# Performance work log

Measured on AMD Instinct MI355X. Metric: run time of the kernel, lower is better.

Reference implementation:

```python
import jax, jax.numpy as jnp
import numpy as np

N = 100000
E = 640000
IN_DIM = 128
HID = 128
NUM_REL = 8


def _rgcn_layer(x, rel_w, root_w, bias, src, dst, edge_type, num_nodes):
    # PyG RGCNConv: out = x @ root + bias + sum_r mean_{edges of rel r into v}(x_src) @ W_r
    out = x @ root_w + bias
    x_src = x[src]  # [E, d_in]
    for r in range(NUM_REL):
        w = (edge_type == r).astype(x.dtype)  # [E]
        msg_sum = jax.ops.segment_sum(x_src * w[:, None], dst, num_segments=num_nodes)
        cnt = jax.ops.segment_sum(w, dst, num_segments=num_nodes)
        agg = msg_sum / jnp.maximum(cnt, 1.0)[:, None]  # mean aggregation per relation
        out = out + agg @ rel_w[r]
    return out


def setup_inputs() -> dict:
    key = jax.random.key(0)
    ks = jax.random.split(key, 10)
    x = jax.random.normal(ks[0], (N, IN_DIM), dtype=jnp.float32)
    edge_index = jax.random.randint(ks[1], (2, E), 0, N, dtype=jnp.int64)
    edge_type = jax.random.randint(ks[2], (E,), 0, NUM_REL, dtype=jnp.int64)
    s1 = 1.0 / np.sqrt(IN_DIM)
    s2 = 1.0 / np.sqrt(HID)
    rel_w1 = jax.random.uniform(ks[3], (NUM_REL, IN_DIM, HID), jnp.float32, -s1, s1)
    root_w1 = jax.random.uniform(ks[4], (IN_DIM, HID), jnp.float32, -s1, s1)
    b1 = jnp.zeros((HID,), jnp.float32)
    rel_w2 = jax.random.uniform(ks[5], (NUM_REL, HID, HID), jnp.float32, -s2, s2)
    root_w2 = jax.random.uniform(ks[6], (HID, HID), jnp.float32, -s2, s2)
    b2 = jnp.zeros((HID,), jnp.float32)
    return {"x": x, "edge_index": edge_index, "edge_type": edge_type,
            "rel_w1": rel_w1, "root_w1": root_w1, "b1": b1,
            "rel_w2": rel_w2, "root_w2": root_w2, "b2": b2}


def reference(x, edge_index, edge_type, rel_w1, root_w1, b1, rel_w2, root_w2, b2):
    src, dst = edge_index[0], edge_index[1]
    h = _rgcn_layer(x, rel_w1, root_w1, b1, src, dst, edge_type, N)
    h = jax.nn.relu(h)  # dropout p=0.0 -> identity
    h = _rgcn_layer(h, rel_w2, root_w2, b2, src, dst, edge_type, N)
    h = jax.nn.relu(h)
    return h
```

## Files before the change

### kernel.cpp

```cpp
#include <hip/hip_runtime.h>
#include <hip/hip_bf16.h>

#define NN 100000
#define EE 640000
#define DD 128
#define RR 8
#define K8 (NN * RR)
#define NSB1 25
#define NSB2 196
#define GBMAX 11571

typedef __attribute__((ext_vector_type(8))) short short8;
typedef __attribute__((ext_vector_type(4))) float floatx4;
typedef __attribute__((ext_vector_type(4))) unsigned int uint4v;

__device__ __forceinline__ unsigned short f2bf(float f) {
  unsigned int u = __float_as_uint(f);
  u += 0x7FFFu + ((u >> 16) & 1u);
  return (unsigned short)(u >> 16);
}
__device__ __forceinline__ unsigned int pk2bf(float a, float b) {
  __hip_bfloat162 h = __float22bfloat162_rn(make_float2(a, b));
  unsigned int u;
  __builtin_memcpy(&u, &h, 4);
  return u;
}
__device__ __forceinline__ float bflo(unsigned int u) { return __uint_as_float(u << 16); }
__device__ __forceinline__ float bfhi(unsigned int u) { return __uint_as_float(u & 0xFFFF0000u); }

__global__ __launch_bounds__(256) void xb_prep(
    const float* __restrict__ x, unsigned int* __restrict__ xb)
{
  int g = blockIdx.x * 256 + threadIdx.x;
  int v = g >> 4, seg = g & 15;
  const float4* s4 = (const float4*)(x + (size_t)v * 128 + seg * 8);
  float4 a = s4[0], b = s4[1];
  uint4v o;
  o[0] = pk2bf(a.x, a.y); o[1] = pk2bf(a.z, a.w);
  o[2] = pk2bf(b.x, b.y); o[3] = pk2bf(b.z, b.w);
  *(uint4v*)(xb + (size_t)v * 64 + seg * 4) = o;
}

__global__ __launch_bounds__(256) void w_prep_all(
    const float* __restrict__ rel1, const float* __restrict__ root1,
    const float* __restrict__ rel2, const float* __restrict__ root2,
    unsigned short* __restrict__ wt)
{
  int id = blockIdx.x * 256 + threadIdx.x;
  int set = id >= 147456;
  int rem = id - set * 147456;
  int r = rem >> 14, n = (rem >> 7) & 127, k = rem & 127;
  const float* rel = set ? rel2 : rel1;
  const float* root = set ? root2 : root1;
  float v = (r < RR) ? rel[((size_t)r * DD + k) * DD + n] : root[(size_t)k * DD + n];
  wt[id] = f2bf(v);
}

__global__ __launch_bounds__(256) void count_all(
    const int* __restrict__ ei, const int* __restrict__ et,
    int* __restrict__ cntd, int* __restrict__ cntdr, int* __restrict__ cntsr)
{
  int e = blockIdx.x * 256 + threadIdx.x;
  int src = ei[e], dst = ei[EE + e], r = et[e];
  atomicAdd(&cntd[dst], 1);
  atomicAdd(&cntdr[dst * RR + r], 1);
  atomicAdd(&cntsr[r * NN + src], 1);
}

__global__ __launch_bounds__(256) void scan_a(
    const int4* __restrict__ c4, int n4, int mode, int* __restrict__ bsum)
{
  int t = threadIdx.x;
  int s = 0;
#pragma unroll
  for (int i = 0; i < 4; ++i) {
    int idx = blockIdx.x * 1024 + i * 256 + t;
    if (idx < n4) {
      int4 v = c4[idx];
      if (mode) s += (v.x > 0) + (v.y > 0) + (v.z > 0) + (v.w > 0);
      else      s += v.x + v.y + v.z + v.w;
    }
  }
  __shared__ int wsum[4];
  for (int d = 32; d; d >>= 1) s += __shfl_xor(s, d, 64);
  if ((t & 63) == 0) wsum[t >> 6] = s;
  __syncthreads();
  if (t == 0) bsum[blockIdx.x] = wsum[0] + wsum[1] + wsum[2] + wsum[3];
}

__global__ void scan_b(const int* __restrict__ bsum, int nsb,
                       int* __restrict__ bbase, int* __restrict__ tot)
{
  int lane = threadIdx.x;
  int v[4]; int s = 0;
#pragma unroll
  for (int i = 0; i < 4; ++i) {
    int idx = lane * 4 + i;
    v[i] = (idx < nsb) ? bsum[idx] : 0; s += v[i];
  }
  int inc = s;
  for (int d = 1; d < 64; d <<= 1) {
    int o = __shfl_up(inc, d, 64);
    if (lane >= d) inc += o;
  }
  int running = inc - s;
#pragma unroll
  for (int i = 0; i < 4; ++i) {
    int idx = lane * 4 + i;
    if (idx < nsb) { bbase[idx] = running; running += v[i]; }
  }
  if (lane == 63 && tot != nullptr) tot[0] = inc;
}

__global__ __launch_bounds__(256) void scan_c(
    const int* __restrict__ cnt, const int* __restrict__ bbase, int n, int mode,
    int* __restrict__ out0, int* __restrict__ out1, int* __restrict__ ubp)
{
  int t = threadIdx.x;
  int base = blockIdx.x * 4096 + t * 16;
  int v[16]; int s = 0;
#pragma unroll
  for (int i = 0; i < 16; ++i) {
    int idx = base + i;
    v[i] = (idx < n) ? cnt[idx] : 0;
    s += mode ? (v[i] > 0) : v[i];
  }
  int lane = t & 63, wid = t >> 6;
  int inc = s;
  for (int d = 1; d < 64; d <<= 1) {
    int o = __shfl_up(inc, d, 64);
    if (lane >= d) inc += o;
  }
  __shared__ int wsum[4];
  if (lane == 63) wsum[wid] = inc;
  __syncthreads();
  int wb = 0;
  for (int w = 0; w < wid; ++w) wb += wsum[w];
  int running = bbase[blockIdx.x] + wb + (inc - s);
#pragma unroll
  for (int i = 0; i < 16; ++i) {
    int idx = base + i;
    if (idx < n) {
      if (mode) {
        if (idx % NN == 0) ubp[idx / NN] = running;
        out0[idx] = (v[i] > 0) ? running : -1;
        running += (v[i] > 0);
      } else {
        out0[idx] = running; out1[idx] = running; running += v[i];
      }
    }
  }
  if (!mode && blockIdx.x == 0 && t == 0) out0[n] = EE;
}

__global__ void pb_kernel(const int* __restrict__ ub, const int* __restrict__ tot,
                          int* __restrict__ pb)
{
  if (threadIdx.x == 0) {
    int base = 0;
    for (int r = 0; r < RR; ++r) {
      pb[r] = base;
      int hi = (r == RR - 1) ? tot[0] : ub[r + 1];
      int u = hi - ub[r];
      base += (u + 63) & ~63;
    }
    pb[8] = base;
    pb[9] = base + ((NN + 63) & ~63);
  }
}

__global__ __launch_bounds__(256) void fix_kernel(
    int* __restrict__ pidx, const int* __restrict__ ub,
    const int* __restrict__ pb, int* __restrict__ ysrc)
{
  int key = blockIdx.x * 256 + threadIdx.x;
  int g = pidx[key];
  if (g < 0) return;
  int r = key / NN, src = key - r * NN;
  int y = pb[r] + (g - ub[r]);
  pidx[key] = y;
  ysrc[y] = src;
}

__global__ __launch_bounds__(256) void place2(
    const int* __restrict__ ei, const int* __restrict__ et,
    const int* __restrict__ cntdr, const int* __restrict__ pidx,
    int* __restrict__ rowfill, int2* __restrict__ recs)
{
  int e = blockIdx.x * 256 + threadIdx.x;
  int src = ei[e], dst = ei[EE + e], r = et[e];
  int slot = atomicAdd(&rowfill[dst], 1);
  float s = 1.0f / (float)max(cntdr[dst * RR + r], 1);
  int2 rec; rec.x = pidx[r * NN + src]; rec.y = __float_as_int(s);
  recs[slot] = rec;
}

__global__ __launch_bounds__(256, 3) void gemm_y(
    const unsigned int* __restrict__ Xb,
    const unsigned short* __restrict__ Wt,
    const int* __restrict__ ysrc,
    const int* __restrict__ pb,
    unsigned int* __restrict__ Ypk)
{
  const int yrow0 = blockIdx.x * 64;
  if (yrow0 >= pb[9]) return;
  int r = 8;
#pragma unroll
  for (int rr = 0; rr < 8; ++rr) if (yrow0 < pb[rr + 1]) { r = rr; break; }

  __shared__ unsigned short As[64 * 128];
  const int tid = threadIdx.x;
  const int wave = tid >> 6, lane = tid & 63;
  const int quad = lane >> 4, mr = lane & 15;
  const int pb8 = pb[8];

  {
    int row = tid >> 2, q = tid & 3;
    int yrow = yrow0 + row;
    int src;
    if (r < RR) src = ysrc[yrow];
    else { src = yrow - pb8; if (src >= NN) src = 0; }
    const uint4v* xs = (const uint4v*)(Xb + (size_t)src * 64 + q * 16);
#pragma unroll
    for (int c = 0; c < 4; ++c) {
      uint4v v = xs[c];
      int pos = (q * 32 + c * 8 + (row & 15) * 8) & 127;
      *(uint4v*)&As[row * 128 + pos] = v;
    }
  }
  const unsigned short* wr = Wt + (size_t)r * 16384 + (size_t)(wave * 32 + mr) * 128 + quad * 8;
  short8 b0[4], b1[4];
#pragma unroll
  for (int ks = 0; ks < 4; ++ks) {
    b0[ks] = *(const short8*)(wr + ks * 32);
    b1[ks] = *(const short8*)(wr + 16 * 128 + ks * 32);
  }
  __syncthreads();

  floatx4 acc[4][2];
#pragma unroll
  for (int mi = 0; mi < 4; ++mi) {
    acc[mi][0] = (floatx4){0.f, 0.f, 0.f, 0.f};
    acc[mi][1] = (floatx4){0.f, 0.f, 0.f, 0.f};
  }
#pragma unroll
  for (int ks = 0; ks < 4; ++ks) {
    short8 a[4];
#pragma unroll
    for (int mi = 0; mi < 4; ++mi)
      a[mi] = *(const short8*)&As[(mi * 16 + mr) * 128 +
                                  ((ks * 32 + quad * 8 + mr * 8) & 127)];
#pragma unroll
    for (int mi = 0; mi < 4; ++mi) {
      acc[mi][0] = __builtin_amdgcn_mfma_f32_16x16x32_bf16(a[mi], b0[ks], acc[mi][0], 0, 0, 0);
      acc[mi][1] = __builtin_amdgcn_mfma_f32_16x16x32_bf16(a[mi], b1[ks], acc[mi][1], 0, 0, 0);
    }
  }
#pragma unroll
  for (int mi = 0; mi < 4; ++mi)
#pragma unroll
    for (int rg = 0; rg < 4; ++rg)
      Ypk[(size_t)(yrow0 + mi * 16 + quad * 4 + rg) * 64 + wave * 16 + mr] =
          pk2bf(acc[mi][0][rg], acc[mi][1][rg]);
}

__global__ __launch_bounds__(256) void aggregate(
    const unsigned int* __restrict__ Ypk,
    const int* __restrict__ rowptr,
    const int2* __restrict__ recs,
    const int* __restrict__ pb,
    const float* __restrict__ bias,
    void* __restrict__ outp, int out_bf16)
{
  int gid = blockIdx.x * 256 + threadIdx.x;
  int v = gid >> 3, o = gid & 7;
  int c0 = 32 * (o >> 1) + 8 * (o & 1);
  int pb8 = pb[8];

  float lo[8], hi[8];
  {
    const uint4v* rp = (const uint4v*)(Ypk + (size_t)(pb8 + v) * 64 + o * 8);
    uint4v u0 = rp[0], u1 = rp[1];
    unsigned um[8];
    *(uint4v*)&um[0] = u0; *(uint4v*)&um[4] = u1;
#pragma unroll
    for (int j = 0; j < 8; ++j) {
      lo[j] = bias[c0 + j] + bflo(um[j]);
      hi[j] = bias[c0 + 16 + j] + bfhi(um[j]);
    }
  }

  int beg = rowptr[v], end = rowptr[v + 1];
  if (beg < end) {
    int2 rec = recs[beg];
    const uint4v* yp = (const uint4v*)(Ypk + (size_t)rec.x * 64 + o * 8);
    uint4v c0v = yp[0], c1v = yp[1];
    for (int e = beg; e < end; ++e) {
      int2 nrec = rec;
      uint4v n0 = c0v, n1 = c1v;
      if (e + 1 < end) {
        nrec = recs[e + 1];
        const uint4v* np = (const uint4v*)(Ypk + (size_t)nrec.x * 64 + o * 8);
        n0 = np[0]; n1 = np[1];
      }
      float s = __int_as_float(rec.y);
      unsigned um[8];
      *(uint4v*)&um[0] = c0v; *(uint4v*)&um[4] = c1v;
#pragma unroll
      for (int j = 0; j < 8; ++j) {
        lo[j] = fmaf(s, bflo(um[j]), lo[j]);
        hi[j] = fmaf(s, bfhi(um[j]), hi[j]);
      }
      rec = nrec; c0v = n0; c1v = n1;
    }
  }

#pragma unroll
  for (int j = 0; j < 8; ++j) {
    lo[j] = fmaxf(lo[j], 0.f);
    hi[j] = fmaxf(hi[j], 0.f);
  }

  if (out_bf16) {
    unsigned int* h = (unsigned int*)outp;
    uint4v wl, wh;
#pragma unroll
    for (int t = 0; t < 4; ++t) {
      wl[t] = pk2bf(lo[2 * t], lo[2 * t + 1]);
      wh[t] = pk2bf(hi[2 * t], hi[2 * t + 1]);
    }
    *(uint4v*)&h[(size_t)v * 64 + c0 / 2] = wl;
    *(uint4v*)&h[(size_t)v * 64 + c0 / 2 + 8] = wh;
  } else {
    float* out = (float*)outp;
    float4* dl = (float4*)(out + (size_t)v * 128 + c0);
    float4* dh = (float4*)(out + (size_t)v * 128 + c0 + 16);
    dl[0] = make_float4(lo[0], lo[1], lo[2], lo[3]);
    dl[1] = make_float4(lo[4], lo[5], lo[6], lo[7]);
    dh[0] = make_float4(hi[0], hi[1], hi[2], hi[3]);
    dh[1] = make_float4(hi[4], hi[5], hi[6], hi[7]);
  }
}

extern "C" void kernel_launch(void* const* d_in, const int* in_sizes, int n_in,
                              void* d_out, int out_size, void* d_ws, size_t ws_size,
                              hipStream_t stream) {
  const float* x       = (const float*)d_in[0];
  const int*   ei      = (const int*)d_in[1];
  const int*   et      = (const int*)d_in[2];
  const float* rel_w1  = (const float*)d_in[3];
  const float* root_w1 = (const float*)d_in[4];
  const float* b1      = (const float*)d_in[5];
  const float* rel_w2  = (const float*)d_in[6];
  const float* root_w2 = (const float*)d_in[7];
  const float* b2      = (const float*)d_in[8];

  char* ws = (char*)d_ws;
  size_t off = 0;
  auto alloc = [&](size_t bytes) { char* p = ws + off; off = (off + bytes + 255) & ~(size_t)255; return p; };
  unsigned int*   Ypk   = (unsigned int*)alloc((size_t)(EE + NN + 1024) * 64 * 4);
  unsigned int*   Xb    = (unsigned int*)alloc((size_t)NN * 64 * 4);
  unsigned int*   h1    = (unsigned int*)alloc((size_t)NN * 64 * 4);
  unsigned short* Wt    = (unsigned short*)alloc((size_t)2 * 9 * DD * DD * 2);
  int*            cntd  = (int*)alloc((size_t)NN * 4);
  int*            cntdr = (int*)alloc((size_t)K8 * 4);
  int*            cntsr = (int*)alloc((size_t)K8 * 4);
  int*            ysrc  = (int*)alloc((size_t)(EE + 1024) * 4);
  char*           zend  = ws + off;
  int*            rowptr= (int*)alloc((size_t)(NN + 1) * 4);
  int*            rowfill=(int*)alloc((size_t)NN * 4);
  int*            pidx  = (int*)alloc((size_t)K8 * 4);
  int2*           recs  = (int2*)alloc((size_t)EE * 8);
  int*            bsum1 = (int*)alloc((size_t)NSB1 * 4);
  int*            bbase1= (int*)alloc((size_t)NSB1 * 4);
  int*            bsum2 = (int*)alloc((size_t)NSB2 * 4);
  int*            bbase2= (int*)alloc((size_t)NSB2 * 4);
  int*            ub    = (int*)alloc(64);
  int*            pb    = (int*)alloc(64);
  int*            Ptot  = (int*)alloc(64);

  hipMemsetAsync(cntd, 0, (size_t)(zend - (char*)cntd), stream);

  xb_prep<<<(NN * 16) / 256, 256, 0, stream>>>(x, Xb);
  w_prep_all<<<(2 * 9 * DD * DD) / 256, 256, 0, stream>>>(rel_w1, root_w1, rel_w2, root_w2, Wt);
  count_all<<<EE / 256, 256, 0, stream>>>(ei, et, cntd, cntdr, cntsr);

  scan_a<<<NSB1, 256, 0, stream>>>((const int4*)cntd, NN / 4, 0, bsum1);
  scan_b<<<1, 64, 0, stream>>>(bsum1, NSB1, bbase1, nullptr);
  scan_c<<<NSB1, 256, 0, stream>>>(cntd, bbase1, NN, 0, rowptr, rowfill, nullptr);

  scan_a<<<NSB2, 256, 0, stream>>>((const int4*)cntsr, K8 / 4, 1, bsum2);
  scan_b<<<1, 64, 0, stream>>>(bsum2, NSB2, bbase2, Ptot);
  scan_c<<<NSB2, 256, 0, stream>>>(cntsr, bbase2, K8, 1, pidx, nullptr, ub);
  pb_kernel<<<1, 64, 0, stream>>>(ub, Ptot, pb);
  fix_kernel<<<K8 / 256, 256, 0, stream>>>(pidx, ub, pb, ysrc);

  place2<<<EE / 256, 256, 0, stream>>>(ei, et, cntdr, pidx, rowfill, recs);

  const int AB = (NN * 8) / 256;

  gemm_y<<<GBMAX, 256, 0, stream>>>(Xb, Wt, ysrc, pb, Ypk);
  aggregate<<<AB, 256, 0, stream>>>(Ypk, rowptr, recs, pb, b1, h1, 1);
  gemm_y<<<GBMAX, 256, 0, stream>>>(h1, Wt + (size_t)9 * DD * DD, ysrc, pb, Ypk);
  aggregate<<<AB, 256, 0, stream>>>(Ypk, rowptr, recs, pb, b2, d_out, 0);
}
```

Baseline: 435.8 us.

## Build per-(dst,rel) CSR via atomic ranks and byte usage flags

The count pass now records each edge's atomic rank within its (dst, relation) bucket and marks used (relation, src) pairs with byte flags, replacing three atomic counters with one atomic plus a plain store. A scan over the dst×relation counts builds a finer row pointer, so edge placement becomes deterministic (offset plus rank) instead of a second atomic pass, and records end up grouped by relation inside each destination row. The usage scan reads packed bytes instead of int counters. In exchange, the destination-count scan grows from 100K to 800K entries and an extra per-edge rank array is written and read.

```diff
diff --git a/kernel.cpp b/kernel.cpp
--- a/kernel.cpp
+++ b/kernel.cpp
@@ -6,7 +6,6 @@
 #define DD 128
 #define RR 8
 #define K8 (NN * RR)
-#define NSB1 25
 #define NSB2 196
 #define GBMAX 11571
 
@@ -58,28 +57,24 @@
 
 __global__ __launch_bounds__(256) void count_all(
     const int* __restrict__ ei, const int* __restrict__ et,
-    int* __restrict__ cntd, int* __restrict__ cntdr, int* __restrict__ cntsr)
+    int* __restrict__ cntdr, unsigned char* __restrict__ used,
+    int* __restrict__ erank)
 {
   int e = blockIdx.x * 256 + threadIdx.x;
   int src = ei[e], dst = ei[EE + e], r = et[e];
-  atomicAdd(&cntd[dst], 1);
-  atomicAdd(&cntdr[dst * RR + r], 1);
-  atomicAdd(&cntsr[r * NN + src], 1);
+  erank[e] = atomicAdd(&cntdr[dst * RR + r], 1);
+  used[r * NN + src] = 1;
 }
 
 __global__ __launch_bounds__(256) void scan_a(
-    const int4* __restrict__ c4, int n4, int mode, int* __restrict__ bsum)
+    const int4* __restrict__ c4, int n4, int* __restrict__ bsum)
 {
   int t = threadIdx.x;
   int s = 0;
 #pragma unroll
   for (int i = 0; i < 4; ++i) {
     int idx = blockIdx.x * 1024 + i * 256 + t;
-    if (idx < n4) {
-      int4 v = c4[idx];
-      if (mode) s += (v.x > 0) + (v.y > 0) + (v.z > 0) + (v.w > 0);
-      else      s += v.x + v.y + v.z + v.w;
-    }
+    if (idx < n4) { int4 v = c4[idx]; s += v.x + v.y + v.z + v.w; }
   }
   __shared__ int wsum[4];
   for (int d = 32; d; d >>= 1) s += __shfl_xor(s, d, 64);
@@ -88,6 +83,28 @@
   if (t == 0) bsum[blockIdx.x] = wsum[0] + wsum[1] + wsum[2] + wsum[3];
 }
 
+__global__ __launch_bounds__(256) void scan_a_u8(
+    const uint4v* __restrict__ c, int n16, int* __restrict__ bsum)
+{
+  int t = threadIdx.x;
+  int idx = blockIdx.x * 256 + t;
+  int s = 0;
+  if (idx < n16) {
+    uint4v v = c[idx];
+#pragma unroll
+    for (int w = 0; w < 4; ++w) {
+      unsigned u = v[w];
+      s += ((u & 0x000000FFu) ? 1 : 0) + ((u & 0x0000FF00u) ? 1 : 0)
+         + ((u & 0x00FF0000u) ? 1 : 0) + ((u & 0xFF000000u) ? 1 : 0);
+    }
+  }
+  __shared__ int wsum[4];
+  for (int d = 32; d; d >>= 1) s += __shfl_xor(s, d, 64);
+  if ((t & 63) == 0) wsum[t >> 6] = s;
+  __syncthreads();
+  if (t == 0) bsum[blockIdx.x] = wsum[0] + wsum[1] + wsum[2] + wsum[3];
+}
+
 __global__ void scan_b(const int* __restrict__ bsum, int nsb,
                        int* __restrict__ bbase, int* __restrict__ tot)
 {
@@ -113,8 +130,8 @@
 }
 
 __global__ __launch_bounds__(256) void scan_c(
-    const int* __restrict__ cnt, const int* __restrict__ bbase, int n, int mode,
-    int* __restrict__ out0, int* __restrict__ out1, int* __restrict__ ubp)
+    const int* __restrict__ cnt, const int* __restrict__ bbase, int n,
+    int* __restrict__ out0)
 {
   int t = threadIdx.x;
   int base = blockIdx.x * 4096 + t * 16;
@@ -123,7 +140,7 @@
   for (int i = 0; i < 16; ++i) {
     int idx = base + i;
     v[i] = (idx < n) ? cnt[idx] : 0;
-    s += mode ? (v[i] > 0) : v[i];
+    s += v[i];
   }
   int lane = t & 63, wid = t >> 6;
   int inc = s;
@@ -140,17 +157,53 @@
 #pragma unroll
   for (int i = 0; i < 16; ++i) {
     int idx = base + i;
+    if (idx < n) { out0[idx] = running; running += v[i]; }
+  }
+  if (blockIdx.x == 0 && t == 0) out0[n] = EE;
+}
+
+__global__ __launch_bounds__(256) void scan_c_u8(
+    const unsigned char* __restrict__ used, const int* __restrict__ bbase, int n,
+    int* __restrict__ out0, int* __restrict__ ubp)
+{
+  int t = threadIdx.x;
+  int base = blockIdx.x * 4096 + t * 16;
+  int v[16]; int s = 0;
+  if (base < n) {
+    uint4v u = *(const uint4v*)(used + base);
+    unsigned um[4]; *(uint4v*)um = u;
+#pragma unroll
+    for (int w = 0; w < 4; ++w)
+#pragma unroll
+      for (int b = 0; b < 4; ++b) {
+        v[w * 4 + b] = ((um[w] >> (8 * b)) & 0xFFu) != 0;
+        s += v[w * 4 + b];
+      }
+  } else {
+#pragma unroll
+    for (int i = 0; i < 16; ++i) v[i] = 0;
+  }
+  int lane = t & 63, wid = t >> 6;
+  int inc = s;
+  for (int d = 1; d < 64; d <<= 1) {
+    int o = __shfl_up(inc, d, 64);
+    if (lane >= d) inc += o;
+  }
+  __shared__ int wsum[4];
+  if (lane == 63) wsum[wid] = inc;
+  __syncthreads();
+  int wb = 0;
+  for (int w = 0; w < wid; ++w) wb += wsum[w];
+  int running = bbase[blockIdx.x] + wb + (inc - s);
+#pragma unroll
+  for (int i = 0; i < 16; ++i) {
+    int idx = base + i;
     if (idx < n) {
-      if (mode) {
-        if (idx % NN == 0) ubp[idx / NN] = running;
-        out0[idx] = (v[i] > 0) ? running : -1;
-        running += (v[i] > 0);
-      } else {
-        out0[idx] = running; out1[idx] = running; running += v[i];
-      }
-    }
-  }
-  if (!mode && blockIdx.x == 0 && t == 0) out0[n] = EE;
+      if (idx % NN == 0) ubp[idx / NN] = running;
+      out0[idx] = v[i] ? running : -1;
+      running += v[i];
+    }
+  }
 }
 
 __global__ void pb_kernel(const int* __restrict__ ub, const int* __restrict__ tot,
@@ -184,13 +237,15 @@
 
 __global__ __launch_bounds__(256) void place2(
     const int* __restrict__ ei, const int* __restrict__ et,
-    const int* __restrict__ cntdr, const int* __restrict__ pidx,
-    int* __restrict__ rowfill, int2* __restrict__ recs)
+    const int* __restrict__ rowptr_dr, const int* __restrict__ pidx,
+    const int* __restrict__ erank, int2* __restrict__ recs)
 {
   int e = blockIdx.x * 256 + threadIdx.x;
   int src = ei[e], dst = ei[EE + e], r = et[e];
-  int slot = atomicAdd(&rowfill[dst], 1);
-  float s = 1.0f / (float)max(cntdr[dst * RR + r], 1);
+  int k = dst * RR + r;
+  int b0 = rowptr_dr[k], b1 = rowptr_dr[k + 1];
+  int slot = b0 + erank[e];
+  float s = 1.0f / (float)max(b1 - b0, 1);
   int2 rec; rec.x = pidx[r * NN + src]; rec.y = __float_as_int(s);
   recs[slot] = rec;
 }
@@ -290,7 +345,7 @@
     }
   }
 
-  int beg = rowptr[v], end = rowptr[v + 1];
+  int beg = rowptr[v * RR], end = rowptr[v * RR + RR];
   if (beg < end) {
     int2 rec = recs[beg];
     const uint4v* yp = (const uint4v*)(Ypk + (size_t)rec.x * 64 + o * 8);
@@ -362,45 +417,44 @@
   unsigned int*   Xb    = (unsigned int*)alloc((size_t)NN * 64 * 4);
   unsigned int*   h1    = (unsigned int*)alloc((size_t)NN * 64 * 4);
   unsigned short* Wt    = (unsigned short*)alloc((size_t)2 * 9 * DD * DD * 2);
-  int*            cntd  = (int*)alloc((size_t)NN * 4);
   int*            cntdr = (int*)alloc((size_t)K8 * 4);
-  int*            cntsr = (int*)alloc((size_t)K8 * 4);
+  unsigned char*  used  = (unsigned char*)alloc((size_t)K8);
   int*            ysrc  = (int*)alloc((size_t)(EE + 1024) * 4);
   char*           zend  = ws + off;
-  int*            rowptr= (int*)alloc((size_t)(NN + 1) * 4);
-  int*            rowfill=(int*)alloc((size_t)NN * 4);
+  int*            rowptr_dr = (int*)alloc((size_t)(K8 + 1) * 4);
+  int*            erank = (int*)alloc((size_t)EE * 4);
   int*            pidx  = (int*)alloc((size_t)K8 * 4);
   int2*           recs  = (int2*)alloc((size_t)EE * 8);
-  int*            bsum1 = (int*)alloc((size_t)NSB1 * 4);
-  int*            bbase1= (int*)alloc((size_t)NSB1 * 4);
-  int*            bsum2 = (int*)alloc((size_t)NSB2 * 4);
-  int*            bbase2= (int*)alloc((size_t)NSB2 * 4);
+  int*            bsumA = (int*)alloc((size_t)NSB2 * 4);
+  int*            bbaseA= (int*)alloc((size_t)NSB2 * 4);
+  int*            bsumB = (int*)alloc((size_t)NSB2 * 4);
+  int*            bbaseB= (int*)alloc((size_t)NSB2 * 4);
   int*            ub    = (int*)alloc(64);
   int*            pb    = (int*)alloc(64);
   int*            Ptot  = (int*)alloc(64);
 
-  hipMemsetAsync(cntd, 0, (size_t)(zend - (char*)cntd), stream);
+  hipMemsetAsync(cntdr, 0, (size_t)(zend - (char*)cntdr), stream);
 
   xb_prep<<<(NN * 16) / 256, 256, 0, stream>>>(x, Xb);
   w_prep_all<<<(2 * 9 * DD * DD) / 256, 256, 0, stream>>>(rel_w1, root_w1, rel_w2, root_w2, Wt);
-  count_all<<<EE / 256, 256, 0, stream>>>(ei, et, cntd, cntdr, cntsr);
-
-  scan_a<<<NSB1, 256, 0, stream>>>((const int4*)cntd, NN / 4, 0, bsum1);
-  scan_b<<<1, 64, 0, stream>>>(bsum1, NSB1, bbase1, nullptr);
-  scan_c<<<NSB1, 256, 0, stream>>>(cntd, bbase1, NN, 0, rowptr, rowfill, nullptr);
-
-  scan_a<<<NSB2, 256, 0, stream>>>((const int4*)cntsr, K8 / 4, 1, bsum2);
-  scan_b<<<1, 64, 0, stream>>>(bsum2, NSB2, bbase2, Ptot);
-  scan_c<<<NSB2, 256, 0, stream>>>(cntsr, bbase2, K8, 1, pidx, nullptr, ub);
+  count_all<<<EE / 256, 256, 0, stream>>>(ei, et, cntdr, used, erank);
+
+  scan_a<<<NSB2, 256, 0, stream>>>((const int4*)cntdr, K8 / 4, bsumA);
+  scan_b<<<1, 64, 0, stream>>>(bsumA, NSB2, bbaseA, nullptr);
+  scan_c<<<NSB2, 256, 0, stream>>>(cntdr, bbaseA, K8, rowptr_dr);
+
+  scan_a_u8<<<NSB2, 256, 0, stream>>>((const uint4v*)used, K8 / 16, bsumB);
+  scan_b<<<1, 64, 0, stream>>>(bsumB, NSB2, bbaseB, Ptot);
+  scan_c_u8<<<NSB2, 256, 0, stream>>>(used, bbaseB, K8, pidx, ub);
   pb_kernel<<<1, 64, 0, stream>>>(ub, Ptot, pb);
   fix_kernel<<<K8 / 256, 256, 0, stream>>>(pidx, ub, pb, ysrc);
 
-  place2<<<EE / 256, 256, 0, stream>>>(ei, et, cntdr, pidx, rowfill, recs);
+  place2<<<EE / 256, 256, 0, stream>>>(ei, et, rowptr_dr, pidx, erank, recs);
 
   const int AB = (NN * 8) / 256;
 
   gemm_y<<<GBMAX, 256, 0, stream>>>(Xb, Wt, ysrc, pb, Ypk);
-  aggregate<<<AB, 256, 0, stream>>>(Ypk, rowptr, recs, pb, b1, h1, 1);
+  aggregate<<<AB, 256, 0, stream>>>(Ypk, rowptr_dr, recs, pb, b1, h1, 1);
   gemm_y<<<GBMAX, 256, 0, stream>>>(h1, Wt + (size_t)9 * DD * DD, ysrc, pb, Ypk);
-  aggregate<<<AB, 256, 0, stream>>>(Ypk, rowptr, recs, pb, b2, d_out, 0);
-}
+  aggregate<<<AB, 256, 0, stream>>>(Ypk, rowptr_dr, recs, pb, b2, d_out, 0);
+}
```

Result: faster. 377.2 us (-13.4%).

## Fuse per-relation mean aggregation with GEMM; aggregate-then-transform per node tile

Applied to the files above, without the earlier changes.

Replaces the transform-then-gather scheme (a GEMM over every unique (relation, source) row into a large Y buffer, then an edge aggregation pass) with one fused kernel per layer. For a tile of 64 destination nodes, that kernel gathers and averages the bf16 source features for each relation into shared memory and multiplies by W_r with MFMA, accumulating all relations plus the root term in registers. The preprocessing becomes a single (relation, dst) CSR built from atomic ranks, which drops several scan, fix and placement kernels along with the large intermediate Y buffer and its traffic. In exchange, the gather is serialized per relation inside each block, there are nine MFMA rounds per tile, and the layer-2 weight rows are permuted to match the h1 bf16 packing.

```diff
diff --git a/kernel.cpp b/kernel.cpp
--- a/kernel.cpp
+++ b/kernel.cpp
@@ -6,9 +6,8 @@
 #define DD 128
 #define RR 8
 #define K8 (NN * RR)
-#define NSB1 25
 #define NSB2 196
-#define GBMAX 11571
+#define NB 1563
 
 typedef __attribute__((ext_vector_type(8))) short short8;
 typedef __attribute__((ext_vector_type(4))) float floatx4;
@@ -50,36 +49,35 @@
   int set = id >= 147456;
   int rem = id - set * 147456;
   int r = rem >> 14, n = (rem >> 7) & 127, k = rem & 127;
+  int kk = k;
+  if (set) {
+    int u = k >> 1, w2 = u >> 4, m2 = u & 15;
+    kk = w2 * 32 + m2 + ((k & 1) << 4);
+  }
   const float* rel = set ? rel2 : rel1;
   const float* root = set ? root2 : root1;
-  float v = (r < RR) ? rel[((size_t)r * DD + k) * DD + n] : root[(size_t)k * DD + n];
+  float v = (r < RR) ? rel[((size_t)r * DD + kk) * DD + n] : root[(size_t)kk * DD + n];
   wt[id] = f2bf(v);
 }
 
 __global__ __launch_bounds__(256) void count_all(
     const int* __restrict__ ei, const int* __restrict__ et,
-    int* __restrict__ cntd, int* __restrict__ cntdr, int* __restrict__ cntsr)
+    int* __restrict__ cnt, int* __restrict__ erank)
 {
   int e = blockIdx.x * 256 + threadIdx.x;
-  int src = ei[e], dst = ei[EE + e], r = et[e];
-  atomicAdd(&cntd[dst], 1);
-  atomicAdd(&cntdr[dst * RR + r], 1);
-  atomicAdd(&cntsr[r * NN + src], 1);
+  int dst = ei[EE + e], r = et[e];
+  erank[e] = atomicAdd(&cnt[r * NN + dst], 1);
 }
 
 __global__ __launch_bounds__(256) void scan_a(
-    const int4* __restrict__ c4, int n4, int mode, int* __restrict__ bsum)
+    const int4* __restrict__ c4, int n4, int* __restrict__ bsum)
 {
   int t = threadIdx.x;
   int s = 0;
 #pragma unroll
   for (int i = 0; i < 4; ++i) {
     int idx = blockIdx.x * 1024 + i * 256 + t;
-    if (idx < n4) {
-      int4 v = c4[idx];
-      if (mode) s += (v.x > 0) + (v.y > 0) + (v.z > 0) + (v.w > 0);
-      else      s += v.x + v.y + v.z + v.w;
-    }
+    if (idx < n4) { int4 v = c4[idx]; s += v.x + v.y + v.z + v.w; }
   }
   __shared__ int wsum[4];
   for (int d = 32; d; d >>= 1) s += __shfl_xor(s, d, 64);
@@ -89,7 +87,7 @@
 }
 
 __global__ void scan_b(const int* __restrict__ bsum, int nsb,
-                       int* __restrict__ bbase, int* __restrict__ tot)
+                       int* __restrict__ bbase)
 {
   int lane = threadIdx.x;
   int v[4]; int s = 0;
@@ -109,12 +107,11 @@
     int idx = lane * 4 + i;
     if (idx < nsb) { bbase[idx] = running; running += v[i]; }
   }
-  if (lane == 63 && tot != nullptr) tot[0] = inc;
 }
 
 __global__ __launch_bounds__(256) void scan_c(
-    const int* __restrict__ cnt, const int* __restrict__ bbase, int n, int mode,
-    int* __restrict__ out0, int* __restrict__ out1, int* __restrict__ ubp)
+    const int* __restrict__ cnt, const int* __restrict__ bbase, int n,
+    int* __restrict__ out0)
 {
   int t = threadIdx.x;
   int base = blockIdx.x * 4096 + t * 16;
@@ -123,7 +120,7 @@
   for (int i = 0; i < 16; ++i) {
     int idx = base + i;
     v[i] = (idx < n) ? cnt[idx] : 0;
-    s += mode ? (v[i] > 0) : v[i];
+    s += v[i];
   }
   int lane = t & 63, wid = t >> 6;
   int inc = s;
@@ -140,102 +137,66 @@
 #pragma unroll
   for (int i = 0; i < 16; ++i) {
     int idx = base + i;
-    if (idx < n) {
-      if (mode) {
-        if (idx % NN == 0) ubp[idx / NN] = running;
-        out0[idx] = (v[i] > 0) ? running : -1;
-        running += (v[i] > 0);
-      } else {
-        out0[idx] = running; out1[idx] = running; running += v[i];
-      }
-    }
-  }
-  if (!mode && blockIdx.x == 0 && t == 0) out0[n] = EE;
-}
-
-__global__ void pb_kernel(const int* __restrict__ ub, const int* __restrict__ tot,
-                          int* __restrict__ pb)
-{
-  if (threadIdx.x == 0) {
-    int base = 0;
-    for (int r = 0; r < RR; ++r) {
-      pb[r] = base;
-      int hi = (r == RR - 1) ? tot[0] : ub[r + 1];
-      int u = hi - ub[r];
-      base += (u + 63) & ~63;
-    }
-    pb[8] = base;
-    pb[9] = base + ((NN + 63) & ~63);
-  }
-}
-
-__global__ __launch_bounds__(256) void fix_kernel(
-    int* __restrict__ pidx, const int* __restrict__ ub,
-    const int* __restrict__ pb, int* __restrict__ ysrc)
-{
-  int key = blockIdx.x * 256 + threadIdx.x;
-  int g = pidx[key];
-  if (g < 0) return;
-  int r = key / NN, src = key - r * NN;
-  int y = pb[r] + (g - ub[r]);
-  pidx[key] = y;
-  ysrc[y] = src;
-}
-
-__global__ __launch_bounds__(256) void place2(
+    if (idx < n) { out0[idx] = running; running += v[i]; }
+  }
+  if (blockIdx.x == 0 && t == 0) out0[n] = EE;
+}
+
+__global__ __launch_bounds__(256) void place(
     const int* __restrict__ ei, const int* __restrict__ et,
-    const int* __restrict__ cntdr, const int* __restrict__ pidx,
-    int* __restrict__ rowfill, int2* __restrict__ recs)
+    const int* __restrict__ rowptr, const int* __restrict__ erank,
+    int* __restrict__ recs)
 {
   int e = blockIdx.x * 256 + threadIdx.x;
   int src = ei[e], dst = ei[EE + e], r = et[e];
-  int slot = atomicAdd(&rowfill[dst], 1);
-  float s = 1.0f / (float)max(cntdr[dst * RR + r], 1);
-  int2 rec; rec.x = pidx[r * NN + src]; rec.y = __float_as_int(s);
-  recs[slot] = rec;
-}
-
-__global__ __launch_bounds__(256, 3) void gemm_y(
+  recs[rowptr[r * NN + dst] + erank[e]] = src;
+}
+
+#define MFMA_ROUND()                                                          \
+  {                                                                           \
+    __syncthreads();                                                          \
+    _Pragma("unroll")                                                         \
+    for (int ks = 0; ks < 4; ++ks) {                                          \
+      short8 a[4];                                                            \
+      _Pragma("unroll")                                                       \
+      for (int mi = 0; mi < 4; ++mi)                                          \
+        a[mi] = *(const short8*)&As[(mi * 16 + mr) * 128 +                    \
+                                    ((ks * 32 + quad * 8 + mr * 8) & 127)];   \
+      _Pragma("unroll")                                                       \
+      for (int mi = 0; mi < 4; ++mi) {                                        \
+        acc[mi][0] = __builtin_amdgcn_mfma_f32_16x16x32_bf16(                 \
+            a[mi], b0[ks], acc[mi][0], 0, 0, 0);                              \
+        acc[mi][1] = __builtin_amdgcn_mfma_f32_16x16x32_bf16(                 \
+            a[mi], b1[ks], acc[mi][1], 0, 0, 0);                              \
+      }                                                                       \
+    }                                                                         \
+    __syncthreads();                                                          \
+  }
+
+__global__ __launch_bounds__(256, 3) void gemm_agg(
     const unsigned int* __restrict__ Xb,
     const unsigned short* __restrict__ Wt,
-    const int* __restrict__ ysrc,
-    const int* __restrict__ pb,
-    unsigned int* __restrict__ Ypk)
-{
-  const int yrow0 = blockIdx.x * 64;
-  if (yrow0 >= pb[9]) return;
-  int r = 8;
-#pragma unroll
-  for (int rr = 0; rr < 8; ++rr) if (yrow0 < pb[rr + 1]) { r = rr; break; }
-
+    const int* __restrict__ rowptr,
+    const int* __restrict__ recs,
+    const float* __restrict__ bias,
+    void* __restrict__ outp, int out_bf16)
+{
+  const int v0 = blockIdx.x * 64;
   __shared__ unsigned short As[64 * 128];
+  __shared__ int Rp[8 * 65];
+
   const int tid = threadIdx.x;
   const int wave = tid >> 6, lane = tid & 63;
   const int quad = lane >> 4, mr = lane & 15;
-  const int pb8 = pb[8];
-
-  {
-    int row = tid >> 2, q = tid & 3;
-    int yrow = yrow0 + row;
-    int src;
-    if (r < RR) src = ysrc[yrow];
-    else { src = yrow - pb8; if (src >= NN) src = 0; }
-    const uint4v* xs = (const uint4v*)(Xb + (size_t)src * 64 + q * 16);
-#pragma unroll
-    for (int c = 0; c < 4; ++c) {
-      uint4v v = xs[c];
-      int pos = (q * 32 + c * 8 + (row & 15) * 8) & 127;
-      *(uint4v*)&As[row * 128 + pos] = v;
-    }
-  }
-  const unsigned short* wr = Wt + (size_t)r * 16384 + (size_t)(wave * 32 + mr) * 128 + quad * 8;
-  short8 b0[4], b1[4];
-#pragma unroll
-  for (int ks = 0; ks < 4; ++ks) {
-    b0[ks] = *(const short8*)(wr + ks * 32);
-    b1[ks] = *(const short8*)(wr + 16 * 128 + ks * 32);
-  }
-  __syncthreads();
+  const int g = lane >> 3, li = lane & 7;
+  const uint4v* Xb4 = (const uint4v*)Xb;
+  unsigned int* Asu = (unsigned int*)As;
+
+  for (int id = tid; id < 520; id += 256) {
+    int r = id / 65, j = id - r * 65;
+    int k = r * NN + v0 + j;
+    Rp[id] = rowptr[min(k, K8)];
+  }
 
   floatx4 acc[4][2];
 #pragma unroll
@@ -243,103 +204,114 @@
     acc[mi][0] = (floatx4){0.f, 0.f, 0.f, 0.f};
     acc[mi][1] = (floatx4){0.f, 0.f, 0.f, 0.f};
   }
-#pragma unroll
-  for (int ks = 0; ks < 4; ++ks) {
-    short8 a[4];
-#pragma unroll
-    for (int mi = 0; mi < 4; ++mi)
-      a[mi] = *(const short8*)&As[(mi * 16 + mr) * 128 +
-                                  ((ks * 32 + quad * 8 + mr * 8) & 127)];
-#pragma unroll
-    for (int mi = 0; mi < 4; ++mi) {
-      acc[mi][0] = __builtin_amdgcn_mfma_f32_16x16x32_bf16(a[mi], b0[ks], acc[mi][0], 0, 0, 0);
-      acc[mi][1] = __builtin_amdgcn_mfma_f32_16x16x32_bf16(a[mi], b1[ks], acc[mi][1], 0, 0, 0);
-    }
-  }
+  __syncthreads();
+
+#pragma unroll 1
+  for (int r = 0; r < 8; ++r) {
+    const unsigned short* wr =
+        Wt + (size_t)r * 16384 + (size_t)(wave * 32 + mr) * 128 + quad * 8;
+    short8 b0[4], b1[4];
+#pragma unroll
+    for (int ks = 0; ks < 4; ++ks) {
+      b0[ks] = *(const short8*)(wr + ks * 32);
+      b1[ks] = *(const short8*)(wr + 16 * 128 + ks * 32);
+    }
+
+#pragma unroll
+    for (int half = 0; half < 2; ++half) {
+      int d = wave * 16 + half * 8 + g;
+      int v = v0 + d;
+      int b = Rp[r * 65 + d];
+      int e = (v < NN) ? Rp[r * 65 + d + 1] : b;
+      int cnt = e - b;
+      int recv = (li < cnt) ? recs[b + li] : 0;
+      float f[16];
+#pragma unroll
+      for (int j = 0; j < 16; ++j) f[j] = 0.f;
+
+      int srcC = __shfl(recv, (g << 3), 64);
+      uint4v u0c{}, u1c{};
+      if (cnt > 0) {
+        const uint4v* xp = Xb4 + (size_t)srcC * 16 + li * 2;
+        u0c = xp[0]; u1c = xp[1];
+      }
+      for (int t = 0; __any(t < cnt); ++t) {
+        int tn = t + 1;
+        int srcN = __shfl(recv, (g << 3) + (tn & 7), 64);
+        bool actN = tn < cnt;
+        if (actN && tn >= 8) srcN = recs[b + tn];
+        uint4v u0n{}, u1n{};
+        if (actN) {
+          const uint4v* xp = Xb4 + (size_t)srcN * 16 + li * 2;
+          u0n = xp[0]; u1n = xp[1];
+        }
+        if (t < cnt) {
+          unsigned um[8];
+          *(uint4v*)&um[0] = u0c; *(uint4v*)&um[4] = u1c;
+#pragma unroll
+          for (int m = 0; m < 8; ++m) {
+            f[2 * m]     += bflo(um[m]);
+            f[2 * m + 1] += bfhi(um[m]);
+          }
+        }
+        u0c = u0n; u1c = u1n;
+      }
+      float sc = 1.0f / (float)max(cnt, 1);
+      int rot = (d & 15) * 4;
+      uint4v o0, o1;
+#pragma unroll
+      for (int m = 0; m < 4; ++m)
+        o0[m] = pk2bf(f[2 * m] * sc, f[2 * m + 1] * sc);
+#pragma unroll
+      for (int m = 0; m < 4; ++m)
+        o1[m] = pk2bf(f[8 + 2 * m] * sc, f[9 + 2 * m] * sc);
+      *(uint4v*)&Asu[d * 64 + ((li * 8 + rot) & 63)] = o0;
+      *(uint4v*)&Asu[d * 64 + ((li * 8 + rot + 4) & 63)] = o1;
+    }
+    MFMA_ROUND();
+  }
+
+  {
+    const unsigned short* wr =
+        Wt + (size_t)8 * 16384 + (size_t)(wave * 32 + mr) * 128 + quad * 8;
+    short8 b0[4], b1[4];
+#pragma unroll
+    for (int ks = 0; ks < 4; ++ks) {
+      b0[ks] = *(const short8*)(wr + ks * 32);
+      b1[ks] = *(const short8*)(wr + 16 * 128 + ks * 32);
+    }
+    int row = tid >> 2, q = tid & 3;
+    int v = v0 + row;
+    int src = (v < NN) ? v : 0;
+    const uint4v* xs = Xb4 + (size_t)src * 16 + q * 4;
+#pragma unroll
+    for (int c = 0; c < 4; ++c) {
+      uint4v vv = xs[c];
+      int pos = (q * 16 + c * 4 + (row & 15) * 4) & 63;
+      *(uint4v*)&Asu[row * 64 + pos] = vv;
+    }
+    MFMA_ROUND();
+  }
+
+  float bia0 = bias[wave * 32 + mr], bia1 = bias[wave * 32 + 16 + mr];
 #pragma unroll
   for (int mi = 0; mi < 4; ++mi)
 #pragma unroll
-    for (int rg = 0; rg < 4; ++rg)
-      Ypk[(size_t)(yrow0 + mi * 16 + quad * 4 + rg) * 64 + wave * 16 + mr] =
-          pk2bf(acc[mi][0][rg], acc[mi][1][rg]);
-}
-
-__global__ __launch_bounds__(256) void aggregate(
-    const unsigned int* __restrict__ Ypk,
-    const int* __restrict__ rowptr,
-    const int2* __restrict__ recs,
-    const int* __restrict__ pb,
-    const float* __restrict__ bias,
-    void* __restrict__ outp, int out_bf16)
-{
-  int gid = blockIdx.x * 256 + threadIdx.x;
-  int v = gid >> 3, o = gid & 7;
-  int c0 = 32 * (o >> 1) + 8 * (o & 1);
-  int pb8 = pb[8];
-
-  float lo[8], hi[8];
-  {
-    const uint4v* rp = (const uint4v*)(Ypk + (size_t)(pb8 + v) * 64 + o * 8);
-    uint4v u0 = rp[0], u1 = rp[1];
-    unsigned um[8];
-    *(uint4v*)&um[0] = u0; *(uint4v*)&um[4] = u1;
-#pragma unroll
-    for (int j = 0; j < 8; ++j) {
-      lo[j] = bias[c0 + j] + bflo(um[j]);
-      hi[j] = bias[c0 + 16 + j] + bfhi(um[j]);
-    }
-  }
-
-  int beg = rowptr[v], end = rowptr[v + 1];
-  if (beg < end) {
-    int2 rec = recs[beg];
-    const uint4v* yp = (const uint4v*)(Ypk + (size_t)rec.x * 64 + o * 8);
-    uint4v c0v = yp[0], c1v = yp[1];
-    for (int e = beg; e < end; ++e) {
-      int2 nrec = rec;
-      uint4v n0 = c0v, n1 = c1v;
-      if (e + 1 < end) {
-        nrec = recs[e + 1];
-        const uint4v* np = (const uint4v*)(Ypk + (size_t)nrec.x * 64 + o * 8);
-        n0 = np[0]; n1 = np[1];
+    for (int rg = 0; rg < 4; ++rg) {
+      int row = mi * 16 + quad * 4 + rg;
+      int v = v0 + row;
+      if (v < NN) {
+        float c0 = fmaxf(acc[mi][0][rg] + bia0, 0.f);
+        float c1 = fmaxf(acc[mi][1][rg] + bia1, 0.f);
+        if (out_bf16) {
+          ((unsigned int*)outp)[(size_t)v * 64 + wave * 16 + mr] = pk2bf(c0, c1);
+        } else {
+          float* o = (float*)outp;
+          o[(size_t)v * 128 + wave * 32 + mr] = c0;
+          o[(size_t)v * 128 + wave * 32 + 16 + mr] = c1;
+        }
       }
-      float s = __int_as_float(rec.y);
-      unsigned um[8];
-      *(uint4v*)&um[0] = c0v; *(uint4v*)&um[4] = c1v;
-#pragma unroll
-      for (int j = 0; j < 8; ++j) {
-        lo[j] = fmaf(s, bflo(um[j]), lo[j]);
-        hi[j] = fmaf(s, bfhi(um[j]), hi[j]);
-      }
-      rec = nrec; c0v = n0; c1v = n1;
-    }
-  }
-
-#pragma unroll
-  for (int j = 0; j < 8; ++j) {
-    lo[j] = fmaxf(lo[j], 0.f);
-    hi[j] = fmaxf(hi[j], 0.f);
-  }
-
-  if (out_bf16) {
-    unsigned int* h = (unsigned int*)outp;
-    uint4v wl, wh;
-#pragma unroll
-    for (int t = 0; t < 4; ++t) {
-      wl[t] = pk2bf(lo[2 * t], lo[2 * t + 1]);
-      wh[t] = pk2bf(hi[2 * t], hi[2 * t + 1]);
-    }
-    *(uint4v*)&h[(size_t)v * 64 + c0 / 2] = wl;
-    *(uint4v*)&h[(size_t)v * 64 + c0 / 2 + 8] = wh;
-  } else {
-    float* out = (float*)outp;
-    float4* dl = (float4*)(out + (size_t)v * 128 + c0);
-    float4* dh = (float4*)(out + (size_t)v * 128 + c0 + 16);
-    dl[0] = make_float4(lo[0], lo[1], lo[2], lo[3]);
-    dl[1] = make_float4(lo[4], lo[5], lo[6], lo[7]);
-    dh[0] = make_float4(hi[0], hi[1], hi[2], hi[3]);
-    dh[1] = make_float4(hi[4], hi[5], hi[6], hi[7]);
-  }
+    }
 }
 
 extern "C" void kernel_launch(void* const* d_in, const int* in_sizes, int n_in,
@@ -358,49 +330,28 @@
   char* ws = (char*)d_ws;
   size_t off = 0;
   auto alloc = [&](size_t bytes) { char* p = ws + off; off = (off + bytes + 255) & ~(size_t)255; return p; };
-  unsigned int*   Ypk   = (unsigned int*)alloc((size_t)(EE + NN + 1024) * 64 * 4);
   unsigned int*   Xb    = (unsigned int*)alloc((size_t)NN * 64 * 4);
   unsigned int*   h1    = (unsigned int*)alloc((size_t)NN * 64 * 4);
   unsigned short* Wt    = (unsigned short*)alloc((size_t)2 * 9 * DD * DD * 2);
-  int*            cntd  = (int*)alloc((size_t)NN * 4);
-  int*            cntdr = (int*)alloc((size_t)K8 * 4);
-  int*            cntsr = (int*)alloc((size_t)K8 * 4);
-  int*            ysrc  = (int*)alloc((size_t)(EE + 1024) * 4);
-  char*           zend  = ws + off;
-  int*            rowptr= (int*)alloc((size_t)(NN + 1) * 4);
-  int*            rowfill=(int*)alloc((size_t)NN * 4);
-  int*            pidx  = (int*)alloc((size_t)K8 * 4);
-  int2*           recs  = (int2*)alloc((size_t)EE * 8);
-  int*            bsum1 = (int*)alloc((size_t)NSB1 * 4);
-  int*            bbase1= (int*)alloc((size_t)NSB1 * 4);
-  int*            bsum2 = (int*)alloc((size_t)NSB2 * 4);
-  int*            bbase2= (int*)alloc((size_t)NSB2 * 4);
-  int*            ub    = (int*)alloc(64);
-  int*            pb    = (int*)alloc(64);
-  int*            Ptot  = (int*)alloc(64);
-
-  hipMemsetAsync(cntd, 0, (size_t)(zend - (char*)cntd), stream);
+  int*            cnt   = (int*)alloc((size_t)K8 * 4);
+  int*            rowptr= (int*)alloc((size_t)(K8 + 1) * 4);
+  int*            erank = (int*)alloc((size_t)EE * 4);
+  int*            recs  = (int*)alloc((size_t)EE * 4);
+  int*            bsum  = (int*)alloc((size_t)NSB2 * 4);
+  int*            bbase = (int*)alloc((size_t)NSB2 * 4);
+
+  hipMemsetAsync(cnt, 0, (size_t)K8 * 4, stream);
 
   xb_prep<<<(NN * 16) / 256, 256, 0, stream>>>(x, Xb);
   w_prep_all<<<(2 * 9 * DD * DD) / 256, 256, 0, stream>>>(rel_w1, root_w1, rel_w2, root_w2, Wt);
-  count_all<<<EE / 256, 256, 0, stream>>>(ei, et, cntd, cntdr, cntsr);
-
-  scan_a<<<NSB1, 256, 0, stream>>>((const int4*)cntd, NN / 4, 0, bsum1);
-  scan_b<<<1, 64, 0, stream>>>(bsum1, NSB1, bbase1, nullptr);
-  scan_c<<<NSB1, 256, 0, stream>>>(cntd, bbase1, NN, 0, rowptr, rowfill, nullptr);
-
-  scan_a<<<NSB2, 256, 0, stream>>>((const int4*)cntsr, K8 / 4, 1, bsum2);
-  scan_b<<<1, 64, 0, stream>>>(bsum2, NSB2, bbase2, Ptot);
-  scan_c<<<NSB2, 256, 0, stream>>>(cntsr, bbase2, K8, 1, pidx, nullptr, ub);
-  pb_kernel<<<1, 64, 0, stream>>>(ub, Ptot, pb);
-  fix_kernel<<<K8 / 256, 256, 0, stream>>>(pidx, ub, pb, ysrc);
-
-  place2<<<EE / 256, 256, 0, stream>>>(ei, et, cntdr, pidx, rowfill, recs);
-
-  const int AB = (NN * 8) / 256;
-
-  gemm_y<<<GBMAX, 256, 0, stream>>>(Xb, Wt, ysrc, pb, Ypk);
-  aggregate<<<AB, 256, 0, stream>>>(Ypk, rowptr, recs, pb, b1, h1, 1);
-  gemm_y<<<GBMAX, 256, 0, stream>>>(h1, Wt + (size_t)9 * DD * DD, ysrc, pb, Ypk);
-  aggregate<<<AB, 256, 0, stream>>>(Ypk, rowptr, recs, pb, b2, d_out, 0);
-}
+  count_all<<<EE / 256, 256, 0, stream>>>(ei, et, cnt, erank);
+
+  scan_a<<<NSB2, 256, 0, stream>>>((const int4*)cnt, K8 / 4, bsum);
+  scan_b<<<1, 64, 0, stream>>>(bsum, NSB2, bbase);
+  scan_c<<<NSB2, 256, 0, stream>>>(cnt, bbase, K8, rowptr);
+
+  place<<<EE / 256, 256, 0, stream>>>(ei, et, rowptr, erank, recs);
+
+  gemm_agg<<<NB, 256, 0, stream>>>(Xb, Wt, rowptr, recs, b1, h1, 1);
+  gemm_agg<<<NB, 256, 0, stream>>>(h1, Wt + (size_t)9 * DD * DD, rowptr, recs, b2, d_out, 0);
+}
```

Result: slower. 495.3 us (+13.6%).
